# Kernel tuning notes

Measured on AMD Instinct MI355X. Metric: run time of the kernel, lower is better.

The kernel has to match this reference:

```python
import jax, jax.numpy as jnp
import numpy as np

H = 64   # LSTM hidden size
NL = 8   # LSTM layers
B, T = 2048, 64


def setup_inputs() -> dict:
    key = jax.random.key(0)
    ks = jax.random.split(key, 18)
    r = lambda i, shape, s=0.1: jax.random.normal(ks[i], shape, dtype=jnp.float32) * s
    return {
        "x": r(0, (B, T, 2), 1.0),
        "w1": r(1, (16, 2)), "b1": r(2, (16,)),
        "w2": r(3, (16, 16)), "b2": r(4, (16,)),
        "w_ih0": r(5, (4 * H, 16)), "w_hh0": r(6, (4 * H, H)),
        "b_ih0": r(7, (4 * H,)), "b_hh0": r(8, (4 * H,)),
        "w_ih": r(9, (NL - 1, 4 * H, H)), "w_hh": r(10, (NL - 1, 4 * H, H)),
        "b_ih": r(11, (NL - 1, 4 * H)), "b_hh": r(12, (NL - 1, 4 * H)),
        "wo1": r(13, (32, H)), "bo1": r(14, (32,)),
        "wo2": r(15, (4, 32)), "bo2": r(16, (4,)),
    }


def _lstm_layer(x, w_ih, w_hh, b):
    # x: [B, T, I]; torch gate order: i, f, g, o
    bsz = x.shape[0]
    xg = jnp.einsum('bti,gi->btg', x, w_ih) + b  # [B, T, 4H] precomputed input gates

    def step(carry, xg_t):
        h, c = carry
        gates = xg_t + h @ w_hh.T
        i, f, g, o = jnp.split(gates, 4, axis=-1)
        i = jax.nn.sigmoid(i); f = jax.nn.sigmoid(f)
        g = jnp.tanh(g); o = jax.nn.sigmoid(o)
        c = f * c + i * g
        h = o * jnp.tanh(c)
        return (h, c), h

    h0 = jnp.zeros((bsz, H), x.dtype)
    _, hs = jax.lax.scan(step, (h0, h0), jnp.swapaxes(xg, 0, 1))  # [T, B, H]
    return jnp.swapaxes(hs, 0, 1)


def reference(x, w1, b1, w2, b2, w_ih0, w_hh0, b_ih0, b_hh0,
              w_ih, w_hh, b_ih, b_hh, wo1, bo1, wo2, bo2):
    # action-input MLP: 2 -> 16 -> relu -> 16
    h = jax.nn.relu(x @ w1.T + b1) @ w2.T + b2
    # 8-layer LSTM, hidden 64
    h = _lstm_layer(h, w_ih0, w_hh0, b_ih0 + b_hh0)
    for l in range(NL - 1):
        h = _lstm_layer(h, w_ih[l], w_hh[l], b_ih[l] + b_hh[l])
    # output MLP: 64 -> 32 -> relu -> 4
    return jax.nn.relu(h @ wo1.T + bo1) @ wo2.T + bo2
```

## Files before the change

### kernel.cpp

```cpp
#include <hip/hip_runtime.h>


#define BATCH 2048
#define TT 64
#define HH 64
#define LDP 136

typedef short bf16x8 __attribute__((ext_vector_type(8)));
typedef float f32x4 __attribute__((ext_vector_type(4)));

__device__ __forceinline__ float sigmoid_fast(float x) {
    return __builtin_amdgcn_rcpf(1.f + __expf(-x));
}
__device__ __forceinline__ float tanh_fast(float x) {
    float e = __expf(-2.f * x);
    e = fminf(e, 1e30f);
    return (1.f - e) * __builtin_amdgcn_rcpf(1.f + e);
}
__device__ __forceinline__ void split2(float x, unsigned short& hi, unsigned short& lo) {
    const unsigned u = __float_as_uint(x);
    hi = (unsigned short)(u >> 16);
    const float r = x - __uint_as_float(u & 0xFFFF0000u);
    lo = (unsigned short)(__float_as_uint(r) >> 16);
}

__global__ __launch_bounds__(256)
void mlp_in_kernel(const float* __restrict__ x,
                   const float* __restrict__ w1, const float* __restrict__ b1,
                   const float* __restrict__ w2, const float* __restrict__ b2,
                   float* __restrict__ out) {
    const int gid = blockIdx.x * 256 + threadIdx.x;
    const float x0 = x[gid * 2 + 0];
    const float x1 = x[gid * 2 + 1];
    float hid[16];
#pragma unroll
    for (int j = 0; j < 16; ++j) {
        float v = fmaf(x1, w1[j * 2 + 1], fmaf(x0, w1[j * 2 + 0], b1[j]));
        hid[j] = fmaxf(0.f, v);
    }
    float o[16];
#pragma unroll
    for (int oo = 0; oo < 16; ++oo) {
        float acc = b2[oo];
#pragma unroll
        for (int j = 0; j < 16; ++j) acc = fmaf(hid[j], w2[oo * 16 + j], acc);
        o[oo] = acc;
    }
    float4* op = (float4*)(out + gid * 16);
#pragma unroll
    for (int q = 0; q < 4; ++q) {
        float4 v;
        v.x = o[q * 4 + 0]; v.y = o[q * 4 + 1]; v.z = o[q * 4 + 2]; v.w = o[q * 4 + 3];
        op[q] = v;
    }
}

template <int IA, int IPADA>
__global__ __launch_bounds__(512, 2)
void lstm_pair(const float* __restrict__ xmlp,
               unsigned* __restrict__ P,
               float* __restrict__ houtf,
               const int last,
               const float* __restrict__ wihA, const float* __restrict__ whhA,
               const float* __restrict__ biA, const float* __restrict__ bhA,
               const float* __restrict__ wihB, const float* __restrict__ whhB,
               const float* __restrict__ biB, const float* __restrict__ bhB) {
    constexpr int KTA = (IPADA + 64) / 32;
    __shared__ unsigned short pAh[2][16 * LDP], pAl[2][16 * LDP];
    __shared__ unsigned short pBh[2][16 * LDP], pBl[2][16 * LDP];

    const int tid = threadIdx.x;
    const int wv = tid >> 6, lane = tid & 63, l16 = lane & 15, quad = lane >> 4;
    const int grp = wv >> 2;
    const int wg = wv & 3;
    const int base = blockIdx.x * 8;

    for (int e = tid; e < 2 * 16 * LDP; e += 512) {
        (&pAh[0][0])[e] = 0; (&pAl[0][0])[e] = 0;
        (&pBh[0][0])[e] = 0; (&pBl[0][0])[e] = 0;
    }

    const int I    = grp ? 64 : IA;
    const int IPAD = grp ? 64 : IPADA;
    const int KT   = grp ? 4  : KTA;
    const float* wih = grp ? wihB : wihA;
    const float* whh = grp ? whhB : whhA;
    const float* bi  = grp ? biB  : biA;
    const float* bh  = grp ? bhB  : bhA;

    const int jg = 16 * wg + l16;
    bf16x8 bhi[4][4], blo[4][4];
    float bsum[4];
#pragma unroll
    for (int gt = 0; gt < 4; ++gt) {
        const int n = gt * 64 + jg;
        bsum[gt] = bi[n] + bh[n];
#pragma unroll
        for (int kt = 0; kt < 4; ++kt) {
            bf16x8 vh = {0, 0, 0, 0, 0, 0, 0, 0};
            bf16x8 vl = {0, 0, 0, 0, 0, 0, 0, 0};
            if (kt < KT) {
#pragma unroll
                for (int j = 0; j < 8; ++j) {
                    const int k = kt * 32 + quad * 8 + j;
                    float w = 0.f;
                    if (k < I) w = wih[n * I + k];
                    else if (k >= IPAD) w = whh[n * 64 + (k - IPAD)];
                    unsigned short h_, l_;
                    split2(w, h_, l_);
                    vh[j] = (short)h_;
                    vl[j] = (short)l_;
                }
            }
            bhi[kt][gt] = vh;
            blo[kt][gt] = vl;
        }
    }

    float cst[4] = {0.f, 0.f, 0.f, 0.f};

    float xrf = 0.f;
    uint2 xru = {0u, 0u};
    int sr = 0, sc = 0;
    if (grp == 0) {
        if (IA == 16) {
            sr = tid >> 4; sc = tid & 15;
            if (tid < 128) {
                xrf = xmlp[((size_t)(base + sr) * TT + 0) * 16 + sc];
                unsigned short h_, l_;
                split2(xrf, h_, l_);
                pAh[0][sr * LDP + sc] = h_;
                pAl[0][sr * LDP + sc] = l_;
                xrf = xmlp[((size_t)(base + sr) * TT + 1) * 16 + sc];
            }
        } else {
            sr = tid >> 5; sc = (tid & 31) * 2;
            xru = *(const uint2*)&P[((size_t)(base + sr) * TT + 0) * 64 + sc];
            pAh[0][sr * LDP + sc + 0] = (unsigned short)(xru.x >> 16);
            pAl[0][sr * LDP + sc + 0] = (unsigned short)(xru.x & 0xffffu);
            pAh[0][sr * LDP + sc + 1] = (unsigned short)(xru.y >> 16);
            pAl[0][sr * LDP + sc + 1] = (unsigned short)(xru.y & 0xffffu);
            xru = *(const uint2*)&P[((size_t)(base + sr) * TT + 1) * 64 + sc];
        }
    }
    __syncthreads();

    for (int s = 0; s <= TT; ++s) {
        if (grp == 0 && s < TT) {
            const int t = s, pb = s & 1;
            f32x4 a0[4], a1[4], a2[4];
#pragma unroll
            for (int gt = 0; gt < 4; ++gt) {
                a0[gt][0] = bsum[gt]; a0[gt][1] = bsum[gt];
                a0[gt][2] = bsum[gt]; a0[gt][3] = bsum[gt];
                a1[gt] = (f32x4){0.f, 0.f, 0.f, 0.f};
                a2[gt] = (f32x4){0.f, 0.f, 0.f, 0.f};
            }
#pragma unroll
            for (int kt = 0; kt < 4; ++kt) {
                if (kt < KTA) {
                    const int aoff = l16 * LDP + kt * 32 + quad * 8;
                    const bf16x8 ahi = *(const bf16x8*)&pAh[pb][aoff];
                    const bf16x8 alo = *(const bf16x8*)&pAl[pb][aoff];
#pragma unroll
                    for (int gt = 0; gt < 4; ++gt) {
                        a0[gt] = __builtin_amdgcn_mfma_f32_16x16x32_bf16(ahi, bhi[kt][gt], a0[gt], 0, 0, 0);
                        a1[gt] = __builtin_amdgcn_mfma_f32_16x16x32_bf16(alo, bhi[kt][gt], a1[gt], 0, 0, 0);
                        a2[gt] = __builtin_amdgcn_mfma_f32_16x16x32_bf16(ahi, blo[kt][gt], a2[gt], 0, 0, 0);
                    }
                }
            }
            if (quad < 2) {
#pragma unroll
                for (int rr = 0; rr < 4; ++rr) {
                    const float gi = (a0[0][rr] + a1[0][rr]) + a2[0][rr];
                    const float gf = (a0[1][rr] + a1[1][rr]) + a2[1][rr];
                    const float gg = (a0[2][rr] + a1[2][rr]) + a2[2][rr];
                    const float go = (a0[3][rr] + a1[3][rr]) + a2[3][rr];
                    const float iv = sigmoid_fast(gi), fv = sigmoid_fast(gf);
                    const float gv = tanh_fast(gg), ov = sigmoid_fast(go);
                    const float cn = fv * cst[rr] + iv * gv;
                    cst[rr] = cn;
                    const float h = ov * tanh_fast(cn);
                    const int R = quad * 4 + rr;
                    unsigned short h_, l_;
                    split2(h, h_, l_);
                    pAh[pb ^ 1][R * LDP + IPADA + jg] = h_;
                    pAl[pb ^ 1][R * LDP + IPADA + jg] = l_;
                    pBh[pb][R * LDP + jg] = h_;
                    pBl[pb][R * LDP + jg] = l_;
                }
            }
            if (IA == 16) {
                if (tid < 128) {
                    unsigned short h_, l_;
                    split2(xrf, h_, l_);
                    pAh[pb ^ 1][sr * LDP + sc] = h_;
                    pAl[pb ^ 1][sr * LDP + sc] = l_;
                    const int tp = (t + 2) & (TT - 1);
                    xrf = xmlp[((size_t)(base + sr) * TT + tp) * 16 + sc];
                }
            } else {
                pAh[pb ^ 1][sr * LDP + sc + 0] = (unsigned short)(xru.x >> 16);
                pAl[pb ^ 1][sr * LDP + sc + 0] = (unsigned short)(xru.x & 0xffffu);
                pAh[pb ^ 1][sr * LDP + sc + 1] = (unsigned short)(xru.y >> 16);
                pAl[pb ^ 1][sr * LDP + sc + 1] = (unsigned short)(xru.y & 0xffffu);
                const int tp = (t + 2) & (TT - 1);
                xru = *(const uint2*)&P[((size_t)(base + sr) * TT + tp) * 64 + sc];
            }
        }

        if (grp == 1 && s >= 1) {
            const int t = s - 1, pb = t & 1;
            f32x4 a0[4], a1[4], a2[4];
#pragma unroll
            for (int gt = 0; gt < 4; ++gt) {
                a0[gt][0] = bsum[gt]; a0[gt][1] = bsum[gt];
                a0[gt][2] = bsum[gt]; a0[gt][3] = bsum[gt];
                a1[gt] = (f32x4){0.f, 0.f, 0.f, 0.f};
                a2[gt] = (f32x4){0.f, 0.f, 0.f, 0.f};
            }
#pragma unroll
            for (int kt = 0; kt < 4; ++kt) {
                const int aoff = l16 * LDP + kt * 32 + quad * 8;
                const bf16x8 ahi = *(const bf16x8*)&pBh[pb][aoff];
                const bf16x8 alo = *(const bf16x8*)&pBl[pb][aoff];
#pragma unroll
                for (int gt = 0; gt < 4; ++gt) {
                    a0[gt] = __builtin_amdgcn_mfma_f32_16x16x32_bf16(ahi, bhi[kt][gt], a0[gt], 0, 0, 0);
                    a1[gt] = __builtin_amdgcn_mfma_f32_16x16x32_bf16(alo, bhi[kt][gt], a1[gt], 0, 0, 0);
                    a2[gt] = __builtin_amdgcn_mfma_f32_16x16x32_bf16(ahi, blo[kt][gt], a2[gt], 0, 0, 0);
                }
            }
            if (quad < 2) {
#pragma unroll
                for (int rr = 0; rr < 4; ++rr) {
                    const float gi = (a0[0][rr] + a1[0][rr]) + a2[0][rr];
                    const float gf = (a0[1][rr] + a1[1][rr]) + a2[1][rr];
                    const float gg = (a0[2][rr] + a1[2][rr]) + a2[2][rr];
                    const float go = (a0[3][rr] + a1[3][rr]) + a2[3][rr];
                    const float iv = sigmoid_fast(gi), fv = sigmoid_fast(gf);
                    const float gv = tanh_fast(gg), ov = sigmoid_fast(go);
                    const float cn = fv * cst[rr] + iv * gv;
                    cst[rr] = cn;
                    const float h = ov * tanh_fast(cn);
                    const int R = quad * 4 + rr;
                    unsigned short h_, l_;
                    split2(h, h_, l_);
                    pBh[pb ^ 1][R * LDP + 64 + jg] = h_;
                    pBl[pb ^ 1][R * LDP + 64 + jg] = l_;
                    if (!last) {
                        P[((size_t)(base + R) * TT + t) * 64 + jg] =
                            ((unsigned)h_ << 16) | (unsigned)l_;
                    } else {
                        houtf[((size_t)(base + R) * TT + t) * HH + jg] = h;
                    }
                }
            }
        }
        __syncthreads();
    }
}

__global__ __launch_bounds__(256)
void mlp_out_kernel(const float* __restrict__ hin,
                    const float* __restrict__ wo1, const float* __restrict__ bo1,
                    const float* __restrict__ wo2, const float* __restrict__ bo2,
                    float* __restrict__ out) {
    __shared__ __align__(16) float wo1_s[32 * 64];
    __shared__ float bo1_s[32];
    __shared__ float wo2_s[4 * 32];
    __shared__ float bo2_s[4];
    const int tid = threadIdx.x;
    for (int e = tid; e < 32 * 64; e += 256) wo1_s[e] = wo1[e];
    if (tid < 32) bo1_s[tid] = bo1[tid];
    if (tid < 128) wo2_s[tid] = wo2[tid];
    if (tid < 4) bo2_s[tid] = bo2[tid];
    __syncthreads();

    const int gid = blockIdx.x * 256 + tid;
    const float4* hv = (const float4*)(hin + gid * 64);
    float4 h[16];
#pragma unroll
    for (int q = 0; q < 16; ++q) h[q] = hv[q];

    float m1[32];
#pragma unroll
    for (int o = 0; o < 32; ++o) {
        float acc = bo1_s[o];
        const float4* wrow = (const float4*)(wo1_s + o * 64);
#pragma unroll
        for (int q = 0; q < 16; ++q) {
            const float4 w = wrow[q];
            acc = fmaf(h[q].x, w.x, acc);
            acc = fmaf(h[q].y, w.y, acc);
            acc = fmaf(h[q].z, w.z, acc);
            acc = fmaf(h[q].w, w.w, acc);
        }
        m1[o] = fmaxf(0.f, acc);
    }
    float r[4];
#pragma unroll
    for (int q = 0; q < 4; ++q) {
        float acc = bo2_s[q];
#pragma unroll
        for (int o = 0; o < 32; ++o) acc = fmaf(m1[o], wo2_s[q * 32 + o], acc);
        r[q] = acc;
    }
    float4 res;
    res.x = r[0]; res.y = r[1]; res.z = r[2]; res.w = r[3];
    ((float4*)out)[gid] = res;
}

extern "C" void kernel_launch(void* const* d_in, const int* in_sizes, int n_in,
                              void* d_out, int out_size, void* d_ws, size_t ws_size,
                              hipStream_t stream) {
    const float* x     = (const float*)d_in[0];
    const float* w1    = (const float*)d_in[1];
    const float* b1    = (const float*)d_in[2];
    const float* w2    = (const float*)d_in[3];
    const float* b2    = (const float*)d_in[4];
    const float* w_ih0 = (const float*)d_in[5];
    const float* w_hh0 = (const float*)d_in[6];
    const float* b_ih0 = (const float*)d_in[7];
    const float* b_hh0 = (const float*)d_in[8];
    const float* w_ih  = (const float*)d_in[9];
    const float* w_hh  = (const float*)d_in[10];
    const float* b_ih  = (const float*)d_in[11];
    const float* b_hh  = (const float*)d_in[12];
    const float* wo1   = (const float*)d_in[13];
    const float* bo1   = (const float*)d_in[14];
    const float* wo2   = (const float*)d_in[15];
    const float* bo2   = (const float*)d_in[16];

    float* buf_mlp = (float*)d_ws;
    unsigned* P = (unsigned*)(buf_mlp + (size_t)BATCH * TT * 16);
    float* bufH = (float*)(P + (size_t)BATCH * TT * 64);

    const int nbt_blocks = (BATCH * TT) / 256;

    mlp_in_kernel<<<nbt_blocks, 256, 0, stream>>>(x, w1, b1, w2, b2, buf_mlp);

    lstm_pair<16, 32><<<BATCH / 8, 512, 0, stream>>>(
        buf_mlp, P, bufH, 0,
        w_ih0, w_hh0, b_ih0, b_hh0,
        w_ih + (size_t)0 * 256 * 64, w_hh + (size_t)0 * 256 * 64, b_ih + 0 * 256, b_hh + 0 * 256);

    for (int p = 1; p < 4; ++p) {
        const int la = 2 * p - 1, lb = 2 * p;
        lstm_pair<64, 64><<<BATCH / 8, 512, 0, stream>>>(
            buf_mlp, P, bufH, (p == 3) ? 1 : 0,
            w_ih + (size_t)la * 256 * 64, w_hh + (size_t)la * 256 * 64,
            b_ih + la * 256, b_hh + la * 256,
            w_ih + (size_t)lb * 256 * 64, w_hh + (size_t)lb * 256 * 64,
            b_ih + lb * 256, b_hh + lb * 256);
    }

    mlp_out_kernel<<<nbt_blocks, 256, 0, stream>>>(bufH, wo1, bo1, wo2, bo2, (float*)d_out);
}
```

Measured before the change: 571.1 us.

## Replace block barriers with LDS counter flags and spread gate math across all lanes

Replaces the per-timestep __syncthreads between the two LSTM layer groups with workgroup-scope atomic counters, so each wave group waits only on the producer steps it actually depends on. This lets layer A run ahead of layer B by up to a step. It also redistributes the gate nonlinearity work through ds_bpermute so all four quads compute two rows each, instead of only half the lanes computing four. The spin-wait with s_sleep adds polling overhead and relies on correct acquire/release ordering of LDS writes across waves.

```diff
diff --git a/kernel.cpp b/kernel.cpp
--- a/kernel.cpp
+++ b/kernel.cpp
@@ -22,6 +22,14 @@
     hi = (unsigned short)(u >> 16);
     const float r = x - __uint_as_float(u & 0xFFFF0000u);
     lo = (unsigned short)(__float_as_uint(r) >> 16);
+}
+__device__ __forceinline__ void wg_wait(int* c, int v) {
+    while (__hip_atomic_load(c, __ATOMIC_ACQUIRE, __HIP_MEMORY_SCOPE_WORKGROUP) < v)
+        __builtin_amdgcn_s_sleep(1);
+}
+__device__ __forceinline__ void wg_bump(int* c, int lane) {
+    if (lane == 0)
+        __hip_atomic_fetch_add(c, 1, __ATOMIC_RELEASE, __HIP_MEMORY_SCOPE_WORKGROUP);
 }
 
 __global__ __launch_bounds__(256)
@@ -68,13 +76,17 @@
     constexpr int KTA = (IPADA + 64) / 32;
     __shared__ unsigned short pAh[2][16 * LDP], pAl[2][16 * LDP];
     __shared__ unsigned short pBh[2][16 * LDP], pBl[2][16 * LDP];
+    __shared__ int cA, cB;
 
     const int tid = threadIdx.x;
     const int wv = tid >> 6, lane = tid & 63, l16 = lane & 15, quad = lane >> 4;
     const int grp = wv >> 2;
     const int wg = wv & 3;
     const int base = blockIdx.x * 8;
-
+    const bool lo32 = (lane < 32);
+    const int bpi = (lane & 31) << 2;
+
+    if (tid == 0) { cA = 0; cB = 0; }
     for (int e = tid; e < 2 * 16 * LDP; e += 512) {
         (&pAh[0][0])[e] = 0; (&pAl[0][0])[e] = 0;
         (&pBh[0][0])[e] = 0; (&pBl[0][0])[e] = 0;
@@ -117,7 +129,8 @@
         }
     }
 
-    float cst[4] = {0.f, 0.f, 0.f, 0.f};
+    float cs[2] = {0.f, 0.f};
+    const int row0 = (quad & 1) * 4 + ((quad >> 1) << 1);
 
     float xrf = 0.f;
     uint2 xru = {0u, 0u};
@@ -145,9 +158,13 @@
     }
     __syncthreads();
 
-    for (int s = 0; s <= TT; ++s) {
-        if (grp == 0 && s < TT) {
-            const int t = s, pb = s & 1;
+    if (grp == 0) {
+        for (int t = 0; t < TT; ++t) {
+            const int pb = t & 1;
+            if (t) {
+                wg_wait(&cA, 4 * t);
+                if (t >= 2) wg_wait(&cB, 4 * (t - 1));
+            }
             f32x4 a0[4], a1[4], a2[4];
 #pragma unroll
             for (int gt = 0; gt < 4; ++gt) {
@@ -157,39 +174,46 @@
                 a2[gt] = (f32x4){0.f, 0.f, 0.f, 0.f};
             }
 #pragma unroll
-            for (int kt = 0; kt < 4; ++kt) {
-                if (kt < KTA) {
-                    const int aoff = l16 * LDP + kt * 32 + quad * 8;
-                    const bf16x8 ahi = *(const bf16x8*)&pAh[pb][aoff];
-                    const bf16x8 alo = *(const bf16x8*)&pAl[pb][aoff];
-#pragma unroll
-                    for (int gt = 0; gt < 4; ++gt) {
-                        a0[gt] = __builtin_amdgcn_mfma_f32_16x16x32_bf16(ahi, bhi[kt][gt], a0[gt], 0, 0, 0);
-                        a1[gt] = __builtin_amdgcn_mfma_f32_16x16x32_bf16(alo, bhi[kt][gt], a1[gt], 0, 0, 0);
-                        a2[gt] = __builtin_amdgcn_mfma_f32_16x16x32_bf16(ahi, blo[kt][gt], a2[gt], 0, 0, 0);
-                    }
-                }
-            }
-            if (quad < 2) {
-#pragma unroll
-                for (int rr = 0; rr < 4; ++rr) {
-                    const float gi = (a0[0][rr] + a1[0][rr]) + a2[0][rr];
-                    const float gf = (a0[1][rr] + a1[1][rr]) + a2[1][rr];
-                    const float gg = (a0[2][rr] + a1[2][rr]) + a2[2][rr];
-                    const float go = (a0[3][rr] + a1[3][rr]) + a2[3][rr];
-                    const float iv = sigmoid_fast(gi), fv = sigmoid_fast(gf);
-                    const float gv = tanh_fast(gg), ov = sigmoid_fast(go);
-                    const float cn = fv * cst[rr] + iv * gv;
-                    cst[rr] = cn;
-                    const float h = ov * tanh_fast(cn);
-                    const int R = quad * 4 + rr;
-                    unsigned short h_, l_;
-                    split2(h, h_, l_);
-                    pAh[pb ^ 1][R * LDP + IPADA + jg] = h_;
-                    pAl[pb ^ 1][R * LDP + IPADA + jg] = l_;
-                    pBh[pb][R * LDP + jg] = h_;
-                    pBl[pb][R * LDP + jg] = l_;
-                }
+            for (int kt = 0; kt < KTA; ++kt) {
+                const int aoff = l16 * LDP + kt * 32 + quad * 8;
+                const bf16x8 ahi = *(const bf16x8*)&pAh[pb][aoff];
+                const bf16x8 alo = *(const bf16x8*)&pAl[pb][aoff];
+#pragma unroll
+                for (int gt = 0; gt < 4; ++gt) {
+                    a0[gt] = __builtin_amdgcn_mfma_f32_16x16x32_bf16(ahi, bhi[kt][gt], a0[gt], 0, 0, 0);
+                    a1[gt] = __builtin_amdgcn_mfma_f32_16x16x32_bf16(alo, bhi[kt][gt], a1[gt], 0, 0, 0);
+                    a2[gt] = __builtin_amdgcn_mfma_f32_16x16x32_bf16(ahi, blo[kt][gt], a2[gt], 0, 0, 0);
+                }
+            }
+            f32x4 s4[4];
+#pragma unroll
+            for (int gt = 0; gt < 4; ++gt) s4[gt] = (a0[gt] + a1[gt]) + a2[gt];
+            float gk[4][2];
+#pragma unroll
+            for (int gt = 0; gt < 4; ++gt) {
+#pragma unroll
+                for (int r = 0; r < 2; ++r) {
+                    const float up = __uint_as_float(
+                        __builtin_amdgcn_ds_bpermute(bpi, __float_as_uint(s4[gt][r + 2])));
+                    gk[gt][r] = lo32 ? s4[gt][r] : up;
+                }
+            }
+#pragma unroll
+            for (int r = 0; r < 2; ++r) {
+                const float iv = sigmoid_fast(gk[0][r]);
+                const float fv = sigmoid_fast(gk[1][r]);
+                const float gv = tanh_fast(gk[2][r]);
+                const float ov = sigmoid_fast(gk[3][r]);
+                const float cn = fv * cs[r] + iv * gv;
+                cs[r] = cn;
+                const float h = ov * tanh_fast(cn);
+                const int R = row0 + r;
+                unsigned short h_, l_;
+                split2(h, h_, l_);
+                pAh[pb ^ 1][R * LDP + IPADA + jg] = h_;
+                pAl[pb ^ 1][R * LDP + IPADA + jg] = l_;
+                pBh[pb][R * LDP + jg] = h_;
+                pBl[pb][R * LDP + jg] = l_;
             }
             if (IA == 16) {
                 if (tid < 128) {
@@ -208,10 +232,13 @@
                 const int tp = (t + 2) & (TT - 1);
                 xru = *(const uint2*)&P[((size_t)(base + sr) * TT + tp) * 64 + sc];
             }
-        }
-
-        if (grp == 1 && s >= 1) {
-            const int t = s - 1, pb = t & 1;
+            wg_bump(&cA, lane);
+        }
+    } else {
+        for (int t = 0; t < TT; ++t) {
+            const int pb = t & 1;
+            wg_wait(&cA, 4 * (t + 1));
+            if (t) wg_wait(&cB, 4 * t);
             f32x4 a0[4], a1[4], a2[4];
 #pragma unroll
             for (int gt = 0; gt < 4; ++gt) {
@@ -232,33 +259,42 @@
                     a2[gt] = __builtin_amdgcn_mfma_f32_16x16x32_bf16(ahi, blo[kt][gt], a2[gt], 0, 0, 0);
                 }
             }
-            if (quad < 2) {
-#pragma unroll
-                for (int rr = 0; rr < 4; ++rr) {
-                    const float gi = (a0[0][rr] + a1[0][rr]) + a2[0][rr];
-                    const float gf = (a0[1][rr] + a1[1][rr]) + a2[1][rr];
-                    const float gg = (a0[2][rr] + a1[2][rr]) + a2[2][rr];
-                    const float go = (a0[3][rr] + a1[3][rr]) + a2[3][rr];
-                    const float iv = sigmoid_fast(gi), fv = sigmoid_fast(gf);
-                    const float gv = tanh_fast(gg), ov = sigmoid_fast(go);
-                    const float cn = fv * cst[rr] + iv * gv;
-                    cst[rr] = cn;
-                    const float h = ov * tanh_fast(cn);
-                    const int R = quad * 4 + rr;
-                    unsigned short h_, l_;
-                    split2(h, h_, l_);
-                    pBh[pb ^ 1][R * LDP + 64 + jg] = h_;
-                    pBl[pb ^ 1][R * LDP + 64 + jg] = l_;
-                    if (!last) {
-                        P[((size_t)(base + R) * TT + t) * 64 + jg] =
-                            ((unsigned)h_ << 16) | (unsigned)l_;
-                    } else {
-                        houtf[((size_t)(base + R) * TT + t) * HH + jg] = h;
-                    }
-                }
-            }
-        }
-        __syncthreads();
+            f32x4 s4[4];
+#pragma unroll
+            for (int gt = 0; gt < 4; ++gt) s4[gt] = (a0[gt] + a1[gt]) + a2[gt];
+            float gk[4][2];
+#pragma unroll
+            for (int gt = 0; gt < 4; ++gt) {
+#pragma unroll
+                for (int r = 0; r < 2; ++r) {
+                    const float up = __uint_as_float(
+                        __builtin_amdgcn_ds_bpermute(bpi, __float_as_uint(s4[gt][r + 2])));
+                    gk[gt][r] = lo32 ? s4[gt][r] : up;
+                }
+            }
+#pragma unroll
+            for (int r = 0; r < 2; ++r) {
+                const float iv = sigmoid_fast(gk[0][r]);
+                const float fv = sigmoid_fast(gk[1][r]);
+                const float gv = tanh_fast(gk[2][r]);
+                const float ov = sigmoid_fast(gk[3][r]);
+                const float cn = fv * cs[r] + iv * gv;
+                cs[r] = cn;
+                const float h = ov * tanh_fast(cn);
+                const int R = row0 + r;
+                unsigned short h_, l_;
+                split2(h, h_, l_);
+                pBh[pb ^ 1][R * LDP + 64 + jg] = h_;
+                pBl[pb ^ 1][R * LDP + 64 + jg] = l_;
+                if (!last) {
+                    P[((size_t)(base + R) * TT + t) * 64 + jg] =
+                        ((unsigned)h_ << 16) | (unsigned)l_;
+                } else {
+                    houtf[((size_t)(base + R) * TT + t) * HH + jg] = h;
+                }
+            }
+            wg_bump(&cB, lane);
+        }
     }
 }
 
```

Measured after the change: 511.3 us. 10.5% less time.
